# Kernel optimization log

Hardware: AMD Instinct MI355X
Metric: run time of the kernel (lower is better)

Reference implementation:

```python
import jax, jax.numpy as jnp
import numpy as np

HIDDEN = 256
NUM_REGIMES = 4

def setup_inputs() -> dict:
    key = jax.random.key(0)
    ks = jax.random.split(key, 9)
    B, D, A = 65536, 256, 128
    x = jax.random.normal(ks[0], (B, D), dtype=jnp.float32)
    regime = jax.random.randint(ks[1], (B,), 0, NUM_REGIMES).astype(jnp.float32)
    x = x.at[:, -1].set(regime)  # last feature holds the discrete regime id
    s1 = 1.0 / np.sqrt(D)
    s2 = 1.0 / np.sqrt(HIDDEN)
    W1 = jax.random.uniform(ks[2], (D, HIDDEN), jnp.float32, -s1, s1)
    b1 = jax.random.uniform(ks[3], (HIDDEN,), jnp.float32, -s1, s1)
    W2 = jax.random.uniform(ks[4], (HIDDEN, HIDDEN), jnp.float32, -s2, s2)
    b2 = jax.random.uniform(ks[5], (HIDDEN,), jnp.float32, -s2, s2)
    Wh = jax.random.uniform(ks[6], (NUM_REGIMES, HIDDEN, A), jnp.float32, -s2, s2)
    bh = jax.random.uniform(ks[7], (NUM_REGIMES, A), jnp.float32, -s2, s2)
    log_std = jnp.zeros((A,), dtype=jnp.float32)
    return {"x": x, "W1": W1, "b1": b1, "W2": W2, "b2": b2,
            "Wh": Wh, "bh": bh, "log_std": log_std}

def reference(x, W1, b1, W2, b2, Wh, bh, log_std):
    # regime index from last feature column (hard routing)
    regime_idx = x[:, -1].astype(jnp.int32)  # [B]
    # backbone MLP: Linear-ReLU-Linear-ReLU
    h = jax.nn.relu(x @ W1 + b1)
    feats = jax.nn.relu(h @ W2 + b2)  # [B, HIDDEN]
    # compute all 4 regime heads densely, then gather per-sample head output
    raw_all = jnp.einsum('bh,rha->bra', feats, Wh) + bh[None, :, :]  # [B, 4, A]
    raw = jnp.take_along_axis(raw_all, regime_idx[:, None, None], axis=1)[:, 0, :]  # [B, A]
    mean = raw * 0.1
    std = jnp.clip(jnp.exp(log_std), 1e-3, 1.0)
    std = jnp.broadcast_to(std[None, :], mean.shape)
    return mean, std
```

## Files before the change

### kernel.cpp

```cpp
#include <hip/hip_runtime.h>
#include <hip/hip_bf16.h>
#include <cstddef>


typedef unsigned short u16;
typedef unsigned int   u32;

using bf16x8 = __attribute__((ext_vector_type(8))) __bf16;
using f32x4  = __attribute__((ext_vector_type(4))) float;

#define BM      64
#define LDSW    264
#define THREADS 512

__device__ __forceinline__ u16 f2bf(float f) {
  return __builtin_bit_cast(u16, (__bf16)f);
}

__global__ void prep_weights(const float* __restrict__ W1,
                             const float* __restrict__ W2,
                             const float* __restrict__ Wh,
                             u16* __restrict__ ws) {
  int i = blockIdx.x * 256 + threadIdx.x;
  {
    int j  = i & 7, l = (i >> 3) & 63, kk = (i >> 9) & 7;
    int nt = (i >> 12) & 1, w = (i >> 13) & 7;
    int n = w * 32 + nt * 16 + (l & 15);
    int k = kk * 32 + ((l >> 4) << 3) + j;
    ws[i]         = f2bf(W1[k * 256 + n]);
    ws[65536 + i] = f2bf(W2[k * 256 + n]);
  }
#pragma unroll
  for (int t = 0; t < 2; ++t) {
    int idx = i + t * 65536;
    int j  = idx & 7, l = (idx >> 3) & 63, kk = (idx >> 9) & 7;
    int ct = (idx >> 12) & 3, w = (idx >> 14) & 7;
    int c = w * 64 + ct * 16 + (l & 15);
    int k = kk * 32 + ((l >> 4) << 3) + j;
    ws[131072 + idx] = f2bf(Wh[(c >> 7) * 32768 + k * 128 + (c & 127)]);
  }
}

__device__ __forceinline__ f32x4 mfma16(bf16x8 a, bf16x8 b, f32x4 c) {
  return __builtin_amdgcn_mfma_f32_16x16x32_bf16(a, b, c, 0, 0, 0);
}

__device__ __forceinline__ void gemm_swapped(const u16* __restrict__ act,
                                             const u16* __restrict__ Wp,
                                             const float* __restrict__ bias,
                                             u16* __restrict__ outbuf,
                                             int w, int ll, int lh, int lane) {
  f32x4 acc[2][4] = {};
#pragma unroll
  for (int kk = 0; kk < 8; ++kk) {
    bf16x8 a[2], b[4];
#pragma unroll
    for (int nt = 0; nt < 2; ++nt)
      a[nt] = *(const bf16x8*)&Wp[((nt * 8 + kk) * 64 + lane) * 8];
#pragma unroll
    for (int bt = 0; bt < 4; ++bt)
      b[bt] = *(const bf16x8*)&act[(bt * 16 + ll) * LDSW + kk * 32 + lh * 8];
#pragma unroll
    for (int nt = 0; nt < 2; ++nt)
#pragma unroll
      for (int bt = 0; bt < 4; ++bt)
        acc[nt][bt] = mfma16(a[nt], b[bt], acc[nt][bt]);
  }
#pragma unroll
  for (int nt = 0; nt < 2; ++nt) {
    const int n0 = w * 32 + nt * 16 + lh * 4;
    const float4 bv = *(const float4*)&bias[n0];
#pragma unroll
    for (int bt = 0; bt < 4; ++bt) {
      ushort4 o;
      o.x = f2bf(fmaxf(acc[nt][bt][0] + bv.x, 0.f));
      o.y = f2bf(fmaxf(acc[nt][bt][1] + bv.y, 0.f));
      o.z = f2bf(fmaxf(acc[nt][bt][2] + bv.z, 0.f));
      o.w = f2bf(fmaxf(acc[nt][bt][3] + bv.w, 0.f));
      *(ushort4*)&outbuf[(bt * 16 + ll) * LDSW + n0] = o;
    }
  }
}

__global__ __launch_bounds__(THREADS, 4) void actor_main(
    const float* __restrict__ x,
    const float* __restrict__ b1, const float* __restrict__ b2,
    const float* __restrict__ bh, const float* __restrict__ log_std,
    const u16* __restrict__ wbf,
    float* __restrict__ out_mean, float* __restrict__ out_std) {
  __shared__ u16 bufX[BM * LDSW];
  __shared__ u16 bufH[BM * LDSW];

  const int tid  = threadIdx.x;
  const int lane = tid & 63;
  const int w    = tid >> 6;
  const int ll   = lane & 15;
  const int lh   = lane >> 4;
  const int row0 = blockIdx.x * BM;

  {
    const float4* xg = (const float4*)(x + (size_t)row0 * 256);
#pragma unroll
    for (int it = 0; it < 8; ++it) {
      const int i = tid + it * THREADS;
      float4 v = xg[i];
      int row = i >> 6, c4 = (i & 63) << 2;
      ushort4 b;
      b.x = f2bf(v.x); b.y = f2bf(v.y); b.z = f2bf(v.z); b.w = f2bf(v.w);
      *(ushort4*)&bufX[row * LDSW + c4] = b;
    }
  }

  {
    const int c4 = (tid & 31) << 2;
    float4 s;
    s.x = fminf(fmaxf(expf(log_std[c4 + 0]), 1e-3f), 1.0f);
    s.y = fminf(fmaxf(expf(log_std[c4 + 1]), 1e-3f), 1.0f);
    s.z = fminf(fmaxf(expf(log_std[c4 + 2]), 1e-3f), 1.0f);
    s.w = fminf(fmaxf(expf(log_std[c4 + 3]), 1e-3f), 1.0f);
#pragma unroll
    for (int i = tid; i < BM * 32; i += THREADS) {
      int row = i >> 5;
      *(float4*)&out_std[(size_t)(row0 + row) * 128 + c4] = s;
    }
  }
  __syncthreads();

  gemm_swapped(bufX, wbf + w * 8192, b1, bufH, w, ll, lh, lane);
  __syncthreads();

  gemm_swapped(bufH, wbf + 65536 + w * 8192, b2, bufX, w, ll, lh, lane);
  __syncthreads();

  {
    const u16* __restrict__ Wp3 = wbf + 131072 + w * 16384;

    int rg[4];
#pragma unroll
    for (int bt = 0; bt < 4; ++bt)
      rg[bt] = (int)x[(size_t)(row0 + bt * 16 + ll) * 256 + 255];

    f32x4 acc[4][4] = {};
#pragma unroll
    for (int kk = 0; kk < 8; ++kk) {
      bf16x8 b[4];
#pragma unroll
      for (int bt = 0; bt < 4; ++bt)
        b[bt] = *(const bf16x8*)&bufX[(bt * 16 + ll) * LDSW + kk * 32 + lh * 8];
#pragma unroll
      for (int ct = 0; ct < 4; ++ct) {
        bf16x8 a = *(const bf16x8*)&Wp3[((ct * 8 + kk) * 64 + lane) * 8];
#pragma unroll
        for (int bt = 0; bt < 4; ++bt)
          acc[ct][bt] = mfma16(a, b[bt], acc[ct][bt]);
      }
    }
    const int head = w >> 1;
#pragma unroll
    for (int ct = 0; ct < 4; ++ct) {
      const int acol = (w & 1) * 64 + ct * 16 + lh * 4;
      const float4 bhv = *(const float4*)&bh[head * 128 + acol];
#pragma unroll
      for (int bt = 0; bt < 4; ++bt) {
        const int brow = bt * 16 + ll;
        if (rg[bt] == head) {
          float4 o;
          o.x = 0.1f * (acc[ct][bt][0] + bhv.x);
          o.y = 0.1f * (acc[ct][bt][1] + bhv.y);
          o.z = 0.1f * (acc[ct][bt][2] + bhv.z);
          o.w = 0.1f * (acc[ct][bt][3] + bhv.w);
          *(float4*)&out_mean[(size_t)(row0 + brow) * 128 + acol] = o;
        }
      }
    }
  }
}

extern "C" void kernel_launch(void* const* d_in, const int* in_sizes, int n_in,
                              void* d_out, int out_size, void* d_ws, size_t ws_size,
                              hipStream_t stream) {
  const float* x  = (const float*)d_in[0];
  const float* W1 = (const float*)d_in[1];
  const float* b1 = (const float*)d_in[2];
  const float* W2 = (const float*)d_in[3];
  const float* b2 = (const float*)d_in[4];
  const float* Wh = (const float*)d_in[5];
  const float* bh = (const float*)d_in[6];
  const float* ls = (const float*)d_in[7];

  const int B = in_sizes[0] / 256;
  float* out_mean = (float*)d_out;
  float* out_std  = out_mean + (size_t)B * 128;
  u16* wbf = (u16*)d_ws;

  hipLaunchKernelGGL(prep_weights, dim3(256), dim3(256), 0, stream, W1, W2, Wh, wbf);
  hipLaunchKernelGGL(actor_main, dim3(B / BM), dim3(THREADS), 0, stream,
                     x, b1, b2, bh, ls, wbf, out_mean, out_std);
}
```

Before: 66.67 us.

## Double block tile to 128 rows with 16 waves and repartition weight layout

Raises rows per block from 64 to 128 and threads from 512 to 1024, so each wave owns 16 output columns in the backbone GEMMs and 32 head columns across two 64-row passes. The weight prep layout is re-derived to match the new per-wave partition. Each weight fragment loaded from global/L2 is now reused across twice as many rows, cutting weight traffic per row, and the block count halves. In exchange LDS use per block doubles (about 135KB), which may limit occupancy to one block per CU. The launch_bounds hint of 4 blocks also cannot be met at this size.

```diff
diff --git a/kernel.cpp b/kernel.cpp
--- a/kernel.cpp
+++ b/kernel.cpp
@@ -9,9 +9,9 @@
 using bf16x8 = __attribute__((ext_vector_type(8))) __bf16;
 using f32x4  = __attribute__((ext_vector_type(4))) float;
 
-#define BM      64
+#define BM      128
 #define LDSW    264
-#define THREADS 512
+#define THREADS 1024
 
 __device__ __forceinline__ u16 f2bf(float f) {
   return __builtin_bit_cast(u16, (__bf16)f);
@@ -24,8 +24,8 @@
   int i = blockIdx.x * 256 + threadIdx.x;
   {
     int j  = i & 7, l = (i >> 3) & 63, kk = (i >> 9) & 7;
-    int nt = (i >> 12) & 1, w = (i >> 13) & 7;
-    int n = w * 32 + nt * 16 + (l & 15);
+    int w  = (i >> 12) & 15;
+    int n = w * 16 + (l & 15);
     int k = kk * 32 + ((l >> 4) << 3) + j;
     ws[i]         = f2bf(W1[k * 256 + n]);
     ws[65536 + i] = f2bf(W2[k * 256 + n]);
@@ -34,8 +34,8 @@
   for (int t = 0; t < 2; ++t) {
     int idx = i + t * 65536;
     int j  = idx & 7, l = (idx >> 3) & 63, kk = (idx >> 9) & 7;
-    int ct = (idx >> 12) & 3, w = (idx >> 14) & 7;
-    int c = w * 64 + ct * 16 + (l & 15);
+    int nb = (idx >> 12) & 1, w = (idx >> 13) & 15;
+    int c = w * 32 + nb * 16 + (l & 15);
     int k = kk * 32 + ((l >> 4) << 3) + j;
     ws[131072 + idx] = f2bf(Wh[(c >> 7) * 32768 + k * 128 + (c & 127)]);
   }
@@ -45,40 +45,33 @@
   return __builtin_amdgcn_mfma_f32_16x16x32_bf16(a, b, c, 0, 0, 0);
 }
 
-__device__ __forceinline__ void gemm_swapped(const u16* __restrict__ act,
-                                             const u16* __restrict__ Wp,
-                                             const float* __restrict__ bias,
-                                             u16* __restrict__ outbuf,
-                                             int w, int ll, int lh, int lane) {
-  f32x4 acc[2][4] = {};
+__device__ __forceinline__ void gemm_swapped16(const u16* __restrict__ act,
+                                               const u16* __restrict__ Wp,
+                                               const float* __restrict__ bias,
+                                               u16* __restrict__ outbuf,
+                                               int w, int ll, int lh, int lane) {
+  f32x4 acc[8] = {};
 #pragma unroll
   for (int kk = 0; kk < 8; ++kk) {
-    bf16x8 a[2], b[4];
+    bf16x8 a = *(const bf16x8*)&Wp[(kk * 64 + lane) * 8];
+    bf16x8 b[8];
 #pragma unroll
-    for (int nt = 0; nt < 2; ++nt)
-      a[nt] = *(const bf16x8*)&Wp[((nt * 8 + kk) * 64 + lane) * 8];
-#pragma unroll
-    for (int bt = 0; bt < 4; ++bt)
+    for (int bt = 0; bt < 8; ++bt)
       b[bt] = *(const bf16x8*)&act[(bt * 16 + ll) * LDSW + kk * 32 + lh * 8];
 #pragma unroll
-    for (int nt = 0; nt < 2; ++nt)
+    for (int bt = 0; bt < 8; ++bt)
+      acc[bt] = mfma16(a, b[bt], acc[bt]);
+  }
+  const int n0 = w * 16 + lh * 4;
+  const float4 bv = *(const float4*)&bias[n0];
 #pragma unroll
-      for (int bt = 0; bt < 4; ++bt)
-        acc[nt][bt] = mfma16(a[nt], b[bt], acc[nt][bt]);
-  }
-#pragma unroll
-  for (int nt = 0; nt < 2; ++nt) {
-    const int n0 = w * 32 + nt * 16 + lh * 4;
-    const float4 bv = *(const float4*)&bias[n0];
-#pragma unroll
-    for (int bt = 0; bt < 4; ++bt) {
-      ushort4 o;
-      o.x = f2bf(fmaxf(acc[nt][bt][0] + bv.x, 0.f));
-      o.y = f2bf(fmaxf(acc[nt][bt][1] + bv.y, 0.f));
-      o.z = f2bf(fmaxf(acc[nt][bt][2] + bv.z, 0.f));
-      o.w = f2bf(fmaxf(acc[nt][bt][3] + bv.w, 0.f));
-      *(ushort4*)&outbuf[(bt * 16 + ll) * LDSW + n0] = o;
-    }
+  for (int bt = 0; bt < 8; ++bt) {
+    ushort4 o;
+    o.x = f2bf(fmaxf(acc[bt][0] + bv.x, 0.f));
+    o.y = f2bf(fmaxf(acc[bt][1] + bv.y, 0.f));
+    o.z = f2bf(fmaxf(acc[bt][2] + bv.z, 0.f));
+    o.w = f2bf(fmaxf(acc[bt][3] + bv.w, 0.f));
+    *(ushort4*)&outbuf[(bt * 16 + ll) * LDSW + n0] = o;
   }
 }
 
@@ -126,50 +119,54 @@
   }
   __syncthreads();
 
-  gemm_swapped(bufX, wbf + w * 8192, b1, bufH, w, ll, lh, lane);
+  gemm_swapped16(bufX, wbf + w * 4096, b1, bufH, w, ll, lh, lane);
   __syncthreads();
 
-  gemm_swapped(bufH, wbf + 65536 + w * 8192, b2, bufX, w, ll, lh, lane);
+  gemm_swapped16(bufH, wbf + 65536 + w * 4096, b2, bufX, w, ll, lh, lane);
   __syncthreads();
 
   {
-    const u16* __restrict__ Wp3 = wbf + 131072 + w * 16384;
+    const u16* __restrict__ Wp3 = wbf + 131072 + w * 8192;
+    const int head = w >> 2;
+#pragma unroll 1
+    for (int p = 0; p < 2; ++p) {
+      const int rbase = p * 64;
 
-    int rg[4];
-#pragma unroll
-    for (int bt = 0; bt < 4; ++bt)
-      rg[bt] = (int)x[(size_t)(row0 + bt * 16 + ll) * 256 + 255];
-
-    f32x4 acc[4][4] = {};
-#pragma unroll
-    for (int kk = 0; kk < 8; ++kk) {
-      bf16x8 b[4];
+      int rg[4];
 #pragma unroll
       for (int bt = 0; bt < 4; ++bt)
-        b[bt] = *(const bf16x8*)&bufX[(bt * 16 + ll) * LDSW + kk * 32 + lh * 8];
+        rg[bt] = (int)x[(size_t)(row0 + rbase + bt * 16 + ll) * 256 + 255];
+
+      f32x4 acc[2][4] = {};
 #pragma unroll
-      for (int ct = 0; ct < 4; ++ct) {
-        bf16x8 a = *(const bf16x8*)&Wp3[((ct * 8 + kk) * 64 + lane) * 8];
+      for (int kk = 0; kk < 8; ++kk) {
+        bf16x8 b[4];
 #pragma unroll
         for (int bt = 0; bt < 4; ++bt)
-          acc[ct][bt] = mfma16(a, b[bt], acc[ct][bt]);
+          b[bt] = *(const bf16x8*)&bufX[(rbase + bt * 16 + ll) * LDSW + kk * 32 + lh * 8];
+#pragma unroll
+        for (int nb = 0; nb < 2; ++nb) {
+          bf16x8 a = *(const bf16x8*)&Wp3[((nb * 8 + kk) * 64 + lane) * 8];
+#pragma unroll
+          for (int bt = 0; bt < 4; ++bt)
+            acc[nb][bt] = mfma16(a, b[bt], acc[nb][bt]);
+        }
       }
-    }
-    const int head = w >> 1;
 #pragma unroll
-    for (int ct = 0; ct < 4; ++ct) {
-      const int acol = (w & 1) * 64 + ct * 16 + lh * 4;
-      const float4 bhv = *(const float4*)&bh[head * 128 + acol];
+      for (int nb = 0; nb < 2; ++nb) {
+        const int acol = (w & 3) * 32 + nb * 16 + lh * 4;
+        const float4 bhv = *(const float4*)&bh[head * 128 + acol];
 #pragma unroll
-      for (int bt = 0; bt < 4; ++bt) {
-        const int brow = bt * 16 + ll;
-        if (rg[bt] == head) {
-          float4 o;
-          o.x = 0.1f * (acc[ct][bt][0] + bhv.x);
-          o.y = 0.1f * (acc[ct][bt][1] + bhv.y);
-          o.z = 0.1f * (acc[ct][bt][2] + bhv.z);
-          o.w = 0.1f * (acc[ct][bt][3] + bhv.w);
-          *(float4*)&out_mean[(size_t)(row0 + brow) * 128 + acol] = o;
+        for (int bt = 0; bt < 4; ++bt) {
+          const int brow = rbase + bt * 16 + ll;
+          if (rg[bt] == head) {
+            float4 o;
+            o.x = 0.1f * (acc[nb][bt][0] + bhv.x);
+            o.y = 0.1f * (acc[nb][bt][1] + bhv.y);
+            o.z = 0.1f * (acc[nb][bt][2] + bhv.z);
+            o.w = 0.1f * (acc[nb][bt][3] + bhv.w);
+            *(float4*)&out_mean[(size_t)(row0 + brow) * 128 + acol] = o;
+          }
         }
       }
     }
```

Result: slower. 69.27 us (+3.9%).
